# Performance work log

Hardware: AMD Instinct MI355X
Metric: run time of the kernel (lower is better)

## Reference

```python
import jax, jax.numpy as jnp
import numpy as np

N = 100000
E = 1600000
F_IN = 64
HEADS = 4
HID = 16
NUM_CLASSES = 2
NEG_SLOPE = 0.2


def setup_inputs() -> dict:
    key = jax.random.key(0)
    ks = jax.random.split(key, 12)
    inputs = jax.random.normal(ks[0], (N, F_IN), dtype=jnp.float32)
    edge_index = jax.random.randint(ks[1], (2, E), 0, N, dtype=jnp.int64)
    edge_attr = jax.random.uniform(ks[2], (E,), dtype=jnp.float32)
    # layer 1 params (GATConv: lin has no bias; final bias of size heads*out)
    s1 = 1.0 / np.sqrt(F_IN)
    W1 = jax.random.uniform(ks[3], (F_IN, HEADS * HID), jnp.float32, -s1, s1)
    att_src1 = jax.random.uniform(ks[4], (HEADS, HID), jnp.float32, -s1, s1)
    att_dst1 = jax.random.uniform(ks[5], (HEADS, HID), jnp.float32, -s1, s1)
    b1 = jnp.zeros((HEADS * HID,), jnp.float32)
    # layer 2 params (heads=1)
    s2 = 1.0 / np.sqrt(HEADS * HID)
    W2 = jax.random.uniform(ks[6], (HEADS * HID, NUM_CLASSES), jnp.float32, -s2, s2)
    att_src2 = jax.random.uniform(ks[7], (1, NUM_CLASSES), jnp.float32, -s2, s2)
    att_dst2 = jax.random.uniform(ks[8], (1, NUM_CLASSES), jnp.float32, -s2, s2)
    b2 = jnp.zeros((NUM_CLASSES,), jnp.float32)
    return {"inputs": inputs, "edge_index": edge_index, "edge_attr": edge_attr,
            "W1": W1, "att_src1": att_src1, "att_dst1": att_dst1, "b1": b1,
            "W2": W2, "att_src2": att_src2, "att_dst2": att_dst2, "b2": b2}


def _add_self_loops(edge_index):
    loop = jnp.arange(N, dtype=edge_index.dtype)
    src = jnp.concatenate([edge_index[0], loop])
    dst = jnp.concatenate([edge_index[1], loop])
    return src, dst


def _gat_layer(x, src, dst, W, a_src, a_dst, bias, heads, out_ch):
    h = (x @ W).reshape(N, heads, out_ch)              # [N,H,C]
    alpha_s = jnp.einsum('nhc,hc->nh', h, a_src)        # [N,H]
    alpha_d = jnp.einsum('nhc,hc->nh', h, a_dst)        # [N,H]
    e = jax.nn.leaky_relu(alpha_s[src] + alpha_d[dst], NEG_SLOPE)  # [E,H]
    # softmax over incoming edges per destination node
    m = jax.ops.segment_max(e, dst, num_segments=N)
    m = jnp.where(jnp.isfinite(m), m, 0.0)
    ex = jnp.exp(e - m[dst])
    denom = jax.ops.segment_sum(ex, dst, num_segments=N)
    alpha = ex / (denom[dst] + 1e-16)                   # [E,H]
    msg = h[src] * alpha[:, :, None]                    # [E,H,C]
    out = jax.ops.segment_sum(msg, dst, num_segments=N) # [N,H,C]
    return out.reshape(N, heads * out_ch) + bias


def reference(inputs, edge_index, edge_attr,
              W1, att_src1, att_dst1, b1,
              W2, att_src2, att_dst2, b2):
    # edge_attr is ignored by GATConv when edge_dim is None (as in the source)
    src, dst = _add_self_loops(edge_index)
    x = _gat_layer(inputs, src, dst, W1, att_src1, att_dst1, b1, HEADS, HID)
    x = jax.nn.relu(x)
    x = _gat_layer(x, src, dst, W2, att_src2, att_dst2, b2, 1, NUM_CLASSES)
    return x
```

## Files before the change

kernel.cpp:

```cpp
#include <hip/hip_runtime.h>
#include <hip/hip_fp16.h>

#define N_NODES 100000
#define NE      1600000
#define ETOT    (NE + N_NODES)
#define F1      64
#define NEG     0.2f
#define CAP     48

#define PBITS   8
#define PSZ     (1 << PBITS)
#define NPART   ((N_NODES + PSZ - 1) / PSZ)
#define N_PAD   (NPART * PSZ)
#define PCAP    5120
#define K2_EPT  8
#define K2_BLK  1024
#define K2_TILE (K2_BLK * K2_EPT)

#define GT      128

static inline int cdiv(int a, int b) { return (a + b - 1) / b; }

__global__ __launch_bounds__(K2_BLK) void partition(
        const int* __restrict__ src, const int* __restrict__ dst,
        int* __restrict__ pcur, int* __restrict__ pairs) {
    __shared__ int hist[NPART];
    __shared__ int base[NPART];
    int t = threadIdx.x;
    for (int i = t; i < NPART; i += K2_BLK) hist[i] = 0;
    __syncthreads();

    int e0 = blockIdx.x * K2_TILE + t;
    int b8[K2_EPT], pos8[K2_EPT], pk8[K2_EPT];
#pragma unroll
    for (int i = 0; i < K2_EPT; ++i) {
        int e = e0 + i * K2_BLK;
        b8[i] = -1;
        if (e < ETOT) {
            int s, d;
            if (e < NE) { s = src[e]; d = dst[e]; } else { s = d = e - NE; }
            int b = d >> PBITS;
            b8[i] = b;
            pk8[i] = ((d & (PSZ - 1)) << 17) | s;
            pos8[i] = atomicAdd(&hist[b], 1);
        }
    }
    __syncthreads();
    for (int i = t; i < NPART; i += K2_BLK)
        base[i] = atomicAdd(&pcur[i], hist[i]);
    __syncthreads();
#pragma unroll
    for (int i = 0; i < K2_EPT; ++i) {
        if (b8[i] >= 0) {
            int idx = base[b8[i]] + pos8[i];
            if (idx < PCAP) pairs[b8[i] * PCAP + idx] = pk8[i];
        }
    }
}

__global__ __launch_bounds__(256) void fine_scatter(
        const int* __restrict__ pcur, const int* __restrict__ pairs,
        int* __restrict__ cnt, int* __restrict__ esrc) {
    __shared__ int lcnt[PSZ];
    int p = blockIdx.x, t = threadIdx.x;
    for (int i = t; i < PSZ; i += 256) lcnt[i] = 0;
    __syncthreads();

    int np = pcur[p];
    np = np < PCAP ? np : PCAP;
    const int* pp = pairs + p * PCAP;
    int nb = p << PBITS;
    for (int i = t; i < np; i += 256) {
        int v = pp[i];
        int ld = v >> 17;
        int s = v & 0x1FFFF;
        int pos = atomicAdd(&lcnt[ld], 1);
        if (pos < CAP) esrc[(size_t)(nb + ld) * CAP + pos] = s;
    }
    __syncthreads();

    for (int i = t; i < PSZ; i += 256)
        if (nb + i < N_NODES) cnt[nb + i] = lcnt[i];
}

__global__ __launch_bounds__(256) void gemm_fused(
        const float* __restrict__ x, const float* __restrict__ W,
        const float* __restrict__ a_src, const float* __restrict__ a_dst,
        __half* __restrict__ h1h, float* __restrict__ as1, float* __restrict__ ad1) {
    __shared__ float sW[64 * 64];
    __shared__ float sXT[64 * 128];
    int t = threadIdx.x;
    int n0 = blockIdx.x * GT;

    for (int i = t; i < 1024; i += 256) ((float4*)sW)[i] = ((const float4*)W)[i];

    for (int i = t; i < 2048; i += 256) {
        int n = i >> 4, kq = i & 15;
        float4 v = make_float4(0.f, 0.f, 0.f, 0.f);
        if (n0 + n < N_NODES) v = ((const float4*)(x + (size_t)(n0 + n) * 64))[kq];
        int k0 = kq * 4, n4 = n >> 2, nl = n & 3;
        sXT[(k0 + 0) * 128 + (((n4 ^ (k0 + 0)) & 31) << 2) + nl] = v.x;
        sXT[(k0 + 1) * 128 + (((n4 ^ (k0 + 1)) & 31) << 2) + nl] = v.y;
        sXT[(k0 + 2) * 128 + (((n4 ^ (k0 + 2)) & 31) << 2) + nl] = v.z;
        sXT[(k0 + 3) * 128 + (((n4 ^ (k0 + 3)) & 31) << 2) + nl] = v.w;
    }
    __syncthreads();

    int jo = t & 7, nq = t >> 3;
    int jo8 = jo * 8;
    float acc[4][8];
#pragma unroll
    for (int m = 0; m < 4; ++m)
#pragma unroll
        for (int c = 0; c < 8; ++c) acc[m][c] = 0.f;

#pragma unroll 4
    for (int k = 0; k < 64; ++k) {
        const float4 xv = *(const float4*)&sXT[k * 128 + (((nq ^ k) & 31) << 2)];
        const float4 w0 = *(const float4*)&sW[k * 64 + jo8];
        const float4 w1 = *(const float4*)&sW[k * 64 + jo8 + 4];
        float xm[4] = {xv.x, xv.y, xv.z, xv.w};
        float wv[8] = {w0.x, w0.y, w0.z, w0.w, w1.x, w1.y, w1.z, w1.w};
#pragma unroll
        for (int m = 0; m < 4; ++m)
#pragma unroll
            for (int c = 0; c < 8; ++c)
                acc[m][c] = fmaf(xm[m], wv[c], acc[m][c]);
    }

    float av[8], dv[8];
#pragma unroll
    for (int c = 0; c < 8; ++c) { av[c] = a_src[jo8 + c]; dv[c] = a_dst[jo8 + c]; }

#pragma unroll
    for (int m = 0; m < 4; ++m) {
        int n = n0 + nq * 4 + m;
        if (n < N_NODES) {
            __half hb[8];
#pragma unroll
            for (int c = 0; c < 8; ++c) hb[c] = __float2half(acc[m][c]);
            *(uint4*)(h1h + (size_t)n * 64 + jo8) = *(const uint4*)hb;
        }
        float ps = 0.f, pd = 0.f;
#pragma unroll
        for (int c = 0; c < 8; ++c) {
            ps = fmaf(acc[m][c], av[c], ps);
            pd = fmaf(acc[m][c], dv[c], pd);
        }
        ps += __shfl_xor(ps, 1, 64);
        pd += __shfl_xor(pd, 1, 64);
        if ((jo & 1) == 0 && n < N_NODES) {
            as1[n * 4 + (jo >> 1)] = ps;
            ad1[n * 4 + (jo >> 1)] = pd;
        }
    }
}

template <int NIT>
__device__ __forceinline__ void rounds(const int* __restrict__ bucket, int deg,
                                       int grp, int sub, int h, float ad,
                                       const __half* __restrict__ h1h,
                                       const float* __restrict__ as1,
                                       float num[8], float& den) {
    int s[NIT];
#pragma unroll
    for (int r = 0; r < NIT; ++r) {
        int ei = r * 8 + grp;
        s[r] = bucket[ei < deg ? ei : 0];
    }
    float a[NIT];
    uint4 g[NIT];
#pragma unroll
    for (int r = 0; r < NIT; ++r) {
        a[r] = as1[s[r] * 4 + h];
        g[r] = *(const uint4*)(h1h + (size_t)s[r] * 64 + sub * 8);
    }
#pragma unroll
    for (int r = 0; r < NIT; ++r) {
        bool act = (r * 8 + grp) < deg;
        float v = a[r] + ad;
        v = v > 0.f ? v : NEG * v;
        float ex = act ? __expf(v) : 0.f;
        const __half2* hp = (const __half2*)&g[r];
#pragma unroll
        for (int q = 0; q < 4; ++q) {
            float2 f = __half22float2(hp[q]);
            num[q * 2 + 0] = fmaf(ex, f.x, num[q * 2 + 0]);
            num[q * 2 + 1] = fmaf(ex, f.y, num[q * 2 + 1]);
        }
        den += ex;
    }
}

__global__ void aggr1(const int* __restrict__ cnt, const int* __restrict__ esrc,
                      const __half* __restrict__ h1h, const float* __restrict__ as1,
                      const float* __restrict__ ad1, const float* __restrict__ b1,
                      const float* __restrict__ W2, const float* __restrict__ a_src2,
                      const float* __restrict__ a_dst2, float4* __restrict__ pack2) {
    int gid = blockIdx.x * blockDim.x + threadIdx.x;
    int w = gid >> 6;
    if (w >= N_NODES) return;
    int lane = threadIdx.x & 63;
    int grp = lane >> 3, sub = lane & 7, h = sub >> 1;
    int deg = cnt[w];
    deg = deg < CAP ? deg : CAP;
    const int* bucket = esrc + (size_t)w * CAP;
    float ad = ad1[w * 4 + h];
    float num[8];
#pragma unroll
    for (int c = 0; c < 8; ++c) num[c] = 0.f;
    float den = 0.f;

    int nit = (deg + 7) >> 3;
    if (nit == 1)      rounds<1>(bucket, deg, grp, sub, h, ad, h1h, as1, num, den);
    else if (nit == 2) rounds<2>(bucket, deg, grp, sub, h, ad, h1h, as1, num, den);
    else if (nit == 3) rounds<3>(bucket, deg, grp, sub, h, ad, h1h, as1, num, den);
    else               rounds<6>(bucket, deg, grp, sub, h, ad, h1h, as1, num, den);

#pragma unroll
    for (int d = 8; d < 64; d <<= 1) {
#pragma unroll
        for (int c = 0; c < 8; ++c) num[c] += __shfl_xor(num[c], d, 64);
        den += __shfl_xor(den, d, 64);
    }
    if (grp == 0) {
        float inv = 1.f / (den + 1e-16f);
        const float4 ba = ((const float4*)b1)[sub * 2];
        const float4 bb = ((const float4*)b1)[sub * 2 + 1];
        float o[8];
        o[0] = fmaf(num[0], inv, ba.x); o[1] = fmaf(num[1], inv, ba.y);
        o[2] = fmaf(num[2], inv, ba.z); o[3] = fmaf(num[3], inv, ba.w);
        o[4] = fmaf(num[4], inv, bb.x); o[5] = fmaf(num[5], inv, bb.y);
        o[6] = fmaf(num[6], inv, bb.z); o[7] = fmaf(num[7], inv, bb.w);
        const float4* w2p = (const float4*)(W2 + sub * 16);
        float4 w2v0 = w2p[0], w2v1 = w2p[1], w2v2 = w2p[2], w2v3 = w2p[3];
        float wtmp[16] = {w2v0.x, w2v0.y, w2v0.z, w2v0.w,
                          w2v1.x, w2v1.y, w2v1.z, w2v1.w,
                          w2v2.x, w2v2.y, w2v2.z, w2v2.w,
                          w2v3.x, w2v3.y, w2v3.z, w2v3.w};
        float p0 = 0.f, p1 = 0.f;
#pragma unroll
        for (int c = 0; c < 8; ++c) {
            float r = fmaxf(o[c], 0.f);
            p0 = fmaf(r, wtmp[c * 2 + 0], p0);
            p1 = fmaf(r, wtmp[c * 2 + 1], p1);
        }
        p0 += __shfl_xor(p0, 1, 64); p1 += __shfl_xor(p1, 1, 64);
        p0 += __shfl_xor(p0, 2, 64); p1 += __shfl_xor(p1, 2, 64);
        p0 += __shfl_xor(p0, 4, 64); p1 += __shfl_xor(p1, 4, 64);
        if (sub == 0) {
            float4 pk;
            pk.x = p0;
            pk.y = p1;
            pk.z = p0 * a_src2[0] + p1 * a_src2[1];
            pk.w = p0 * a_dst2[0] + p1 * a_dst2[1];
            pack2[w] = pk;
        }
    }
}

__global__ void aggr2(const int* __restrict__ cnt, const int* __restrict__ esrc,
                      const float4* __restrict__ pack2, const float* __restrict__ b2,
                      float* __restrict__ out) {
    int gid = blockIdx.x * blockDim.x + threadIdx.x;
    int node = gid >> 4;
    if (node >= N_NODES) return;
    int sub = threadIdx.x & 15;
    int deg = cnt[node];
    deg = deg < CAP ? deg : CAP;
    const int* bucket = esrc + (size_t)node * CAP;
    float adv = pack2[node].w;

    int e1 = 16 + sub, e2 = 32 + sub;
    int s0 = bucket[sub < deg ? sub : 0];
    int s1 = bucket[e1 < deg ? e1 : 0];
    int s2 = bucket[e2 < deg ? e2 : 0];
    float4 q0 = pack2[s0];
    float4 q1 = pack2[s1];
    float4 q2 = pack2[s2];

    float v0 = q0.z + adv; v0 = v0 > 0.f ? v0 : NEG * v0;
    float v1 = q1.z + adv; v1 = v1 > 0.f ? v1 : NEG * v1;
    float v2 = q2.z + adv; v2 = v2 > 0.f ? v2 : NEG * v2;
    float x0 = (sub < deg) ? __expf(v0) : 0.f;
    float x1 = (e1 < deg) ? __expf(v1) : 0.f;
    float x2 = (e2 < deg) ? __expf(v2) : 0.f;

    float n0 = x0 * q0.x + x1 * q1.x + x2 * q2.x;
    float n1 = x0 * q0.y + x1 * q1.y + x2 * q2.y;
    float den = x0 + x1 + x2;
#pragma unroll
    for (int d = 1; d < 16; d <<= 1) {
        n0  += __shfl_xor(n0, d, 64);
        n1  += __shfl_xor(n1, d, 64);
        den += __shfl_xor(den, d, 64);
    }
    if (sub == 0) {
        float inv = 1.f / (den + 1e-16f);
        float2 o;
        o.x = fmaf(n0, inv, b2[0]);
        o.y = fmaf(n1, inv, b2[1]);
        *(float2*)(out + node * 2) = o;
    }
}

extern "C" void kernel_launch(void* const* d_in, const int* in_sizes, int n_in,
                              void* d_out, int out_size, void* d_ws, size_t ws_size,
                              hipStream_t stream) {
    const float* x        = (const float*)d_in[0];
    const int*   ei       = (const int*)d_in[1];
    const float* W1       = (const float*)d_in[3];
    const float* att_src1 = (const float*)d_in[4];
    const float* att_dst1 = (const float*)d_in[5];
    const float* b1       = (const float*)d_in[6];
    const float* W2       = (const float*)d_in[7];
    const float* att_src2 = (const float*)d_in[8];
    const float* att_dst2 = (const float*)d_in[9];
    const float* b2       = (const float*)d_in[10];

    const int* src = ei;
    const int* dst = ei + NE;
    float* out = (float*)d_out;

    char* p = (char*)d_ws;
    int* pcur     = (int*)p;     p += sizeof(int) * 512;
    int* cnt      = (int*)p;     p += sizeof(int) * N_NODES;
    int* esrc     = (int*)p;     p += sizeof(int) * (size_t)N_PAD * CAP;
    __half* h1h   = (__half*)p;  p += sizeof(__half) * (size_t)N_NODES * F1;
    float* as1    = (float*)p;   p += sizeof(float) * N_NODES * 4;
    float* ad1    = (float*)p;   p += sizeof(float) * N_NODES * 4;
    float4* pack2 = (float4*)p;  p += sizeof(float4) * N_NODES;
    int* pairs    = (int*)p;     p += sizeof(int) * (size_t)NPART * PCAP;

    const int B = 256;

    hipMemsetAsync(pcur, 0, sizeof(int) * 512, stream);
    partition<<<cdiv(ETOT, K2_TILE), K2_BLK, 0, stream>>>(src, dst, pcur, pairs);
    fine_scatter<<<NPART, 256, 0, stream>>>(pcur, pairs, cnt, esrc);
    gemm_fused<<<cdiv(N_NODES, GT), 256, 0, stream>>>(x, W1, att_src1, att_dst1,
                                                      h1h, as1, ad1);
    aggr1<<<cdiv(N_NODES * 64, B), B, 0, stream>>>(cnt, esrc, h1h, as1, ad1, b1,
                                                   W2, att_src2, att_dst2, pack2);
    aggr2<<<cdiv(N_NODES * 16, B), B, 0, stream>>>(cnt, esrc, pack2, b2, out);
}
```

Baseline: 203.3 us.

## Merge fine scatter and GEMM into one launch, skip empty aggr2 rounds

Folds the fine_scatter and gemm_fused kernels into a single launch. Block index decides which role a block takes, and a shared-memory union holds the separate scratch buffers. This removes one kernel launch and lets the two independent stages overlap on the GPU. The partition tile is halved (4 edges per thread instead of 8), which roughly doubles the number of partition blocks. In aggr2, the second and third 16-edge rounds now run only when some lane's node degree exceeds 16 or 32, avoiding loads and exp work for low-degree nodes at the cost of wave-level branches.

```diff
diff --git a/kernel.cpp b/kernel.cpp
--- a/kernel.cpp
+++ b/kernel.cpp
@@ -13,11 +13,12 @@
 #define NPART   ((N_NODES + PSZ - 1) / PSZ)
 #define N_PAD   (NPART * PSZ)
 #define PCAP    5120
-#define K2_EPT  8
+#define K2_EPT  4
 #define K2_BLK  1024
 #define K2_TILE (K2_BLK * K2_EPT)
 
 #define GT      128
+#define NGB     ((N_NODES + GT - 1) / GT)
 
 static inline int cdiv(int a, int b) { return (a + b - 1) / b; }
 
@@ -31,18 +32,18 @@
     __syncthreads();
 
     int e0 = blockIdx.x * K2_TILE + t;
-    int b8[K2_EPT], pos8[K2_EPT], pk8[K2_EPT];
+    int b4[K2_EPT], pos4[K2_EPT], pk4[K2_EPT];
 #pragma unroll
     for (int i = 0; i < K2_EPT; ++i) {
         int e = e0 + i * K2_BLK;
-        b8[i] = -1;
+        b4[i] = -1;
         if (e < ETOT) {
             int s, d;
             if (e < NE) { s = src[e]; d = dst[e]; } else { s = d = e - NE; }
             int b = d >> PBITS;
-            b8[i] = b;
-            pk8[i] = ((d & (PSZ - 1)) << 17) | s;
-            pos8[i] = atomicAdd(&hist[b], 1);
+            b4[i] = b;
+            pk4[i] = ((d & (PSZ - 1)) << 17) | s;
+            pos4[i] = atomicAdd(&hist[b], 1);
         }
     }
     __syncthreads();
@@ -51,58 +52,60 @@
     __syncthreads();
 #pragma unroll
     for (int i = 0; i < K2_EPT; ++i) {
-        if (b8[i] >= 0) {
-            int idx = base[b8[i]] + pos8[i];
-            if (idx < PCAP) pairs[b8[i] * PCAP + idx] = pk8[i];
-        }
-    }
-}
-
-__global__ __launch_bounds__(256) void fine_scatter(
+        if (b4[i] >= 0) {
+            int idx = base[b4[i]] + pos4[i];
+            if (idx < PCAP) pairs[b4[i] * PCAP + idx] = pk4[i];
+        }
+    }
+}
+
+__global__ __launch_bounds__(256) void fs_gemm(
         const int* __restrict__ pcur, const int* __restrict__ pairs,
-        int* __restrict__ cnt, int* __restrict__ esrc) {
-    __shared__ int lcnt[PSZ];
-    int p = blockIdx.x, t = threadIdx.x;
-    for (int i = t; i < PSZ; i += 256) lcnt[i] = 0;
-    __syncthreads();
-
-    int np = pcur[p];
-    np = np < PCAP ? np : PCAP;
-    const int* pp = pairs + p * PCAP;
-    int nb = p << PBITS;
-    for (int i = t; i < np; i += 256) {
-        int v = pp[i];
-        int ld = v >> 17;
-        int s = v & 0x1FFFF;
-        int pos = atomicAdd(&lcnt[ld], 1);
-        if (pos < CAP) esrc[(size_t)(nb + ld) * CAP + pos] = s;
-    }
-    __syncthreads();
-
-    for (int i = t; i < PSZ; i += 256)
-        if (nb + i < N_NODES) cnt[nb + i] = lcnt[i];
-}
-
-__global__ __launch_bounds__(256) void gemm_fused(
+        int* __restrict__ cnt, int* __restrict__ esrc,
         const float* __restrict__ x, const float* __restrict__ W,
         const float* __restrict__ a_src, const float* __restrict__ a_dst,
         __half* __restrict__ h1h, float* __restrict__ as1, float* __restrict__ ad1) {
-    __shared__ float sW[64 * 64];
-    __shared__ float sXT[64 * 128];
+    __shared__ union {
+        int lcnt[PSZ];
+        struct { float sW[64 * 64]; float sXT[64 * 128]; } g;
+    } u;
     int t = threadIdx.x;
-    int n0 = blockIdx.x * GT;
-
-    for (int i = t; i < 1024; i += 256) ((float4*)sW)[i] = ((const float4*)W)[i];
+
+    if (blockIdx.x < NPART) {
+        int p = blockIdx.x;
+        for (int i = t; i < PSZ; i += 256) u.lcnt[i] = 0;
+        __syncthreads();
+        int np = pcur[p];
+        np = np < PCAP ? np : PCAP;
+        const int* pp = pairs + p * PCAP;
+        int nb = p << PBITS;
+        for (int i = t; i < np; i += 256) {
+            int v = pp[i];
+            int ld = v >> 17;
+            int s = v & 0x1FFFF;
+            int pos = atomicAdd(&u.lcnt[ld], 1);
+            if (pos < CAP) esrc[(size_t)(nb + ld) * CAP + pos] = s;
+        }
+        __syncthreads();
+        for (int i = t; i < PSZ; i += 256)
+            if (nb + i < N_NODES) cnt[nb + i] = u.lcnt[i];
+        return;
+    }
+
+    int n0 = (blockIdx.x - NPART) * GT;
+
+    for (int i = t; i < 1024; i += 256)
+        ((float4*)u.g.sW)[i] = ((const float4*)W)[i];
 
     for (int i = t; i < 2048; i += 256) {
         int n = i >> 4, kq = i & 15;
         float4 v = make_float4(0.f, 0.f, 0.f, 0.f);
         if (n0 + n < N_NODES) v = ((const float4*)(x + (size_t)(n0 + n) * 64))[kq];
         int k0 = kq * 4, n4 = n >> 2, nl = n & 3;
-        sXT[(k0 + 0) * 128 + (((n4 ^ (k0 + 0)) & 31) << 2) + nl] = v.x;
-        sXT[(k0 + 1) * 128 + (((n4 ^ (k0 + 1)) & 31) << 2) + nl] = v.y;
-        sXT[(k0 + 2) * 128 + (((n4 ^ (k0 + 2)) & 31) << 2) + nl] = v.z;
-        sXT[(k0 + 3) * 128 + (((n4 ^ (k0 + 3)) & 31) << 2) + nl] = v.w;
+        u.g.sXT[(k0 + 0) * 128 + (((n4 ^ (k0 + 0)) & 31) << 2) + nl] = v.x;
+        u.g.sXT[(k0 + 1) * 128 + (((n4 ^ (k0 + 1)) & 31) << 2) + nl] = v.y;
+        u.g.sXT[(k0 + 2) * 128 + (((n4 ^ (k0 + 2)) & 31) << 2) + nl] = v.z;
+        u.g.sXT[(k0 + 3) * 128 + (((n4 ^ (k0 + 3)) & 31) << 2) + nl] = v.w;
     }
     __syncthreads();
 
@@ -116,9 +119,9 @@
 
 #pragma unroll 4
     for (int k = 0; k < 64; ++k) {
-        const float4 xv = *(const float4*)&sXT[k * 128 + (((nq ^ k) & 31) << 2)];
-        const float4 w0 = *(const float4*)&sW[k * 64 + jo8];
-        const float4 w1 = *(const float4*)&sW[k * 64 + jo8 + 4];
+        const float4 xv = *(const float4*)&u.g.sXT[k * 128 + (((nq ^ k) & 31) << 2)];
+        const float4 w0 = *(const float4*)&u.g.sW[k * 64 + jo8];
+        const float4 w1 = *(const float4*)&u.g.sW[k * 64 + jo8 + 4];
         float xm[4] = {xv.x, xv.y, xv.z, xv.w};
         float wv[8] = {w0.x, w0.y, w0.z, w0.w, w1.x, w1.y, w1.z, w1.w};
 #pragma unroll
@@ -271,24 +274,28 @@
     const int* bucket = esrc + (size_t)node * CAP;
     float adv = pack2[node].w;
 
-    int e1 = 16 + sub, e2 = 32 + sub;
     int s0 = bucket[sub < deg ? sub : 0];
-    int s1 = bucket[e1 < deg ? e1 : 0];
-    int s2 = bucket[e2 < deg ? e2 : 0];
     float4 q0 = pack2[s0];
-    float4 q1 = pack2[s1];
-    float4 q2 = pack2[s2];
-
     float v0 = q0.z + adv; v0 = v0 > 0.f ? v0 : NEG * v0;
-    float v1 = q1.z + adv; v1 = v1 > 0.f ? v1 : NEG * v1;
-    float v2 = q2.z + adv; v2 = v2 > 0.f ? v2 : NEG * v2;
     float x0 = (sub < deg) ? __expf(v0) : 0.f;
-    float x1 = (e1 < deg) ? __expf(v1) : 0.f;
-    float x2 = (e2 < deg) ? __expf(v2) : 0.f;
-
-    float n0 = x0 * q0.x + x1 * q1.x + x2 * q2.x;
-    float n1 = x0 * q0.y + x1 * q1.y + x2 * q2.y;
-    float den = x0 + x1 + x2;
+    float n0 = x0 * q0.x, n1 = x0 * q0.y, den = x0;
+
+    if (__any(deg > 16)) {
+        int e1 = 16 + sub;
+        int s1 = bucket[e1 < deg ? e1 : 0];
+        float4 q1 = pack2[s1];
+        float v1 = q1.z + adv; v1 = v1 > 0.f ? v1 : NEG * v1;
+        float x1 = (e1 < deg) ? __expf(v1) : 0.f;
+        n0 = fmaf(x1, q1.x, n0); n1 = fmaf(x1, q1.y, n1); den += x1;
+    }
+    if (__any(deg > 32)) {
+        int e2 = 32 + sub;
+        int s2 = bucket[e2 < deg ? e2 : 0];
+        float4 q2 = pack2[s2];
+        float v2 = q2.z + adv; v2 = v2 > 0.f ? v2 : NEG * v2;
+        float x2 = (e2 < deg) ? __expf(v2) : 0.f;
+        n0 = fmaf(x2, q2.x, n0); n1 = fmaf(x2, q2.y, n1); den += x2;
+    }
 #pragma unroll
     for (int d = 1; d < 16; d <<= 1) {
         n0  += __shfl_xor(n0, d, 64);
@@ -336,9 +343,9 @@
 
     hipMemsetAsync(pcur, 0, sizeof(int) * 512, stream);
     partition<<<cdiv(ETOT, K2_TILE), K2_BLK, 0, stream>>>(src, dst, pcur, pairs);
-    fine_scatter<<<NPART, 256, 0, stream>>>(pcur, pairs, cnt, esrc);
-    gemm_fused<<<cdiv(N_NODES, GT), 256, 0, stream>>>(x, W1, att_src1, att_dst1,
-                                                      h1h, as1, ad1);
+    fs_gemm<<<NPART + NGB, 256, 0, stream>>>(pcur, pairs, cnt, esrc,
+                                             x, W1, att_src1, att_dst1,
+                                             h1h, as1, ad1);
     aggr1<<<cdiv(N_NODES * 64, B), B, 0, stream>>>(cnt, esrc, h1h, as1, ad1, b1,
                                                    W2, att_src2, att_dst2, pack2);
     aggr2<<<cdiv(N_NODES * 16, B), B, 0, stream>>>(cnt, esrc, pack2, b2, out);
```

Result: slower. 207.5 us (+2.0%).
